# Optimization experiments

Measured on AMD Instinct MI355X. Metric: run time of the kernel, lower is better.

## Reference

```python
import jax, jax.numpy as jnp
import numpy as np

LATENT_DIM = 128
KQ_DIM = 32
B, N, K = 4, 16384, 64


def setup_inputs() -> dict:
    key = jax.random.key(0)
    k1, k2, k3, k4, k5, k6, k7 = jax.random.split(key, 7)
    return {
        "indices": jax.random.randint(k1, (3, B, N, K), 0, N, dtype=jnp.int64)
        if jax.config.jax_enable_x64 else jax.random.randint(k1, (3, B, N, K), 0, N, dtype=jnp.int32),
        "img": jax.random.normal(k2, (B, 3, 128, 128), dtype=jnp.float32),
        "features": jax.random.normal(k3, (B, N, LATENT_DIM), dtype=jnp.float32),
        "Wk": jax.random.normal(k4, (KQ_DIM, LATENT_DIM), dtype=jnp.float32) * 0.05,
        "bk": jax.random.normal(k5, (KQ_DIM,), dtype=jnp.float32) * 0.05,
        "Wq": jax.random.normal(k6, (KQ_DIM, LATENT_DIM), dtype=jnp.float32) * 0.05,
        "bq": jax.random.normal(k7, (KQ_DIM,), dtype=jnp.float32) * 0.05,
    }


def reference(indices, img, features, Wk, bk, Wq, bq):
    # features: [B, N, latent] -> keys/queries: [B, N, D]
    ks = jnp.einsum("bnl,dl->bnd", features, Wk) + bk
    qs = jnp.einsum("bnl,dl->bnd", features, Wq) + bq
    D = ks.shape[-1]
    # indices row 1 indexes keys, row 2 indexes queries (values in [0, N))
    x_idx = indices[1].reshape(B, N * K)  # [B, N*K]
    y_idx = indices[2].reshape(B, N * K)
    # gather along node axis: [B, N*K, D]
    x_feat = jnp.take_along_axis(ks, x_idx[:, :, None], axis=1)
    y_feat = jnp.take_along_axis(qs, y_idx[:, :, None], axis=1)
    # scaled dot product per edge -> [B, N, K]
    logits = (x_feat * y_feat).sum(axis=-1).reshape(B, N, K) * (D ** -0.5)
    return logits
```

## Files before the change

kernel.cpp:

```cpp
#include <hip/hip_runtime.h>
#include <hip/hip_fp16.h>

#define LATENT 128
#define DQK    32
#define BB     4
#define NN     16384
#define KK     64
#define TOTAL_EDGES (BB * NN * KK)
#define TOTAL_NODES (BB * NN)
#define PAD    132

__global__ __launch_bounds__(256, 2) void proj_kernel(
    const float* __restrict__ features,
    const float* __restrict__ Wk,
    const float* __restrict__ bk,
    const float* __restrict__ Wq,
    const float* __restrict__ bq,
    __half* __restrict__ ks,
    __half* __restrict__ qs)
{
    __shared__ float sf[64 * PAD];
    __shared__ float sw[64 * PAD];
    __shared__ float sb[64];

    const int t = threadIdx.x;
    const int node0 = blockIdx.x * 64;

    #pragma unroll
    for (int j = 0; j < 8; ++j) {
        int idx = t + j * 256;
        int r = idx >> 5;
        int c = idx & 31;
        const float4* src = (r < 32) ? (const float4*)Wk : (const float4*)Wq;
        float4 v = src[(size_t)(r & 31) * 32 + c];
        *(float4*)&sw[r * PAD + c * 4] = v;
    }
    if (t < 64) sb[t] = (t < 32) ? bk[t] : bq[t - 32];

    #pragma unroll
    for (int j = 0; j < 8; ++j) {
        int idx = t + j * 256;
        int r = idx >> 5;
        int c = idx & 31;
        float4 v = ((const float4*)(features + (size_t)(node0 + r) * LATENT))[c];
        *(float4*)&sf[r * PAD + c * 4] = v;
    }
    __syncthreads();

    const int tx = t & 15;
    const int ty = t >> 4;

    float acc[4][4];
    #pragma unroll
    for (int i = 0; i < 4; ++i)
        #pragma unroll
        for (int u = 0; u < 4; ++u) acc[i][u] = 0.f;

    #pragma unroll 4
    for (int kk = 0; kk < 32; ++kk) {
        float4 a[4], b[4];
        #pragma unroll
        for (int i = 0; i < 4; ++i)
            a[i] = *(const float4*)&sf[(ty * 4 + i) * PAD + kk * 4];
        #pragma unroll
        for (int u = 0; u < 4; ++u)
            b[u] = *(const float4*)&sw[(tx + 16 * u) * PAD + kk * 4];
        #pragma unroll
        for (int i = 0; i < 4; ++i)
            #pragma unroll
            for (int u = 0; u < 4; ++u)
                acc[i][u] += a[i].x * b[u].x + a[i].y * b[u].y
                           + a[i].z * b[u].z + a[i].w * b[u].w;
    }

    #pragma unroll
    for (int u = 0; u < 4; ++u) {
        const int d = tx + 16 * u;
        const float bias = sb[d];
        __half* base = (d < 32) ? ks : qs;
        const int dd = d & 31;
        #pragma unroll
        for (int i = 0; i < 4; ++i) {
            const int node = node0 + ty * 4 + i;
            base[(size_t)node * DQK + dd] = __float2half(acc[i][u] + bias);
        }
    }
}

__device__ __forceinline__ float dot8_h(uint4 a, uint4 b) {
    const __half2* ah = (const __half2*)&a;
    const __half2* bh = (const __half2*)&b;
    float s = 0.f;
    #pragma unroll
    for (int i = 0; i < 4; ++i) {
        const float2 af = __half22float2(ah[i]);
        const float2 bf = __half22float2(bh[i]);
        s += af.x * bf.x + af.y * bf.y;
    }
    return s;
}

__global__ __launch_bounds__(256) void edge_kernel(
    const int* __restrict__ xidx,
    const int* __restrict__ yidx,
    const __half* __restrict__ ks,
    const __half* __restrict__ qs,
    float* __restrict__ out)
{
    const int t = blockIdx.x * 256 + threadIdx.x;
    const int e = t >> 2;
    const int j = t & 3;
    const int b = e >> 20;

    const int x = xidx[e];
    const int y = yidx[e];

    const uint4 kv = ((const uint4*)ks)[((size_t)((b << 14) + x)) * 4 + j];
    const uint4 qv = ((const uint4*)qs)[((size_t)((b << 14) + y)) * 4 + j];

    float acc = dot8_h(kv, qv);
    acc += __shfl_xor(acc, 1);
    acc += __shfl_xor(acc, 2);

    if (j == 0) out[e] = acc * 0.17677669529663687f;
}

extern "C" void kernel_launch(void* const* d_in, const int* in_sizes, int n_in,
                              void* d_out, int out_size, void* d_ws, size_t ws_size,
                              hipStream_t stream) {
    const int*   indices  = (const int*)d_in[0];
    const float* features = (const float*)d_in[2];
    const float* Wk       = (const float*)d_in[3];
    const float* bk       = (const float*)d_in[4];
    const float* Wq       = (const float*)d_in[5];
    const float* bq       = (const float*)d_in[6];
    float* out = (float*)d_out;

    __half* ks = (__half*)d_ws;
    __half* qs = ks + (size_t)TOTAL_NODES * DQK;

    const int* xidx = indices + (size_t)1 * TOTAL_EDGES;
    const int* yidx = indices + (size_t)2 * TOTAL_EDGES;

    proj_kernel<<<TOTAL_NODES / 64, 256, 0, stream>>>(features, Wk, bk, Wq, bq, ks, qs);
    edge_kernel<<<(TOTAL_EDGES * 4) / 256, 256, 0, stream>>>(xidx, yidx, ks, qs, out);
}
```

Before: 74.12 us.

## Compute edge dot products with MFMA diagonal, one wave per 64 edges

Replaces the 4-threads-per-edge shuffle reduction with a 16x16x32 f16 MFMA per group of 16 edges, extracting the diagonal entries as the dot products. Each wave processes 64 edges in four unrolled groups, cutting launched threads by four and removing shuffles and conversions. It wastes most of the matrix product and adds a per-lane select, and fewer threads may hide gather latency less well.

```diff
diff --git a/kernel.cpp b/kernel.cpp
--- a/kernel.cpp
+++ b/kernel.cpp
@@ -9,6 +9,9 @@
 #define TOTAL_EDGES (BB * NN * KK)
 #define TOTAL_NODES (BB * NN)
 #define PAD    132
+
+typedef _Float16 half8 __attribute__((ext_vector_type(8)));
+typedef float    f32x4 __attribute__((ext_vector_type(4)));
 
 __global__ __launch_bounds__(256, 2) void proj_kernel(
     const float* __restrict__ features,
@@ -87,19 +90,6 @@
     }
 }
 
-__device__ __forceinline__ float dot8_h(uint4 a, uint4 b) {
-    const __half2* ah = (const __half2*)&a;
-    const __half2* bh = (const __half2*)&b;
-    float s = 0.f;
-    #pragma unroll
-    for (int i = 0; i < 4; ++i) {
-        const float2 af = __half22float2(ah[i]);
-        const float2 bf = __half22float2(bh[i]);
-        s += af.x * bf.x + af.y * bf.y;
-    }
-    return s;
-}
-
 __global__ __launch_bounds__(256) void edge_kernel(
     const int* __restrict__ xidx,
     const int* __restrict__ yidx,
@@ -107,22 +97,39 @@
     const __half* __restrict__ qs,
     float* __restrict__ out)
 {
-    const int t = blockIdx.x * 256 + threadIdx.x;
-    const int e = t >> 2;
-    const int j = t & 3;
-    const int b = e >> 20;
+    const int lane = threadIdx.x & 63;
+    const int wave = (blockIdx.x * 256 + threadIdx.x) >> 6;
+    const int i = lane & 15;
+    const int c = lane >> 4;
+    const int e_base = wave * 64;
+    const int b = e_base >> 20;
+    const int nodebase = b << 14;
 
-    const int x = xidx[e];
-    const int y = yidx[e];
+    const _Float16* ksh = (const _Float16*)ks;
+    const _Float16* qsh = (const _Float16*)qs;
 
-    const uint4 kv = ((const uint4*)ks)[((size_t)((b << 14) + x)) * 4 + j];
-    const uint4 qv = ((const uint4*)qs)[((size_t)((b << 14) + y)) * 4 + j];
+    const bool writer = (c == (i >> 2));
+    const int reg = i & 3;
 
-    float acc = dot8_h(kv, qv);
-    acc += __shfl_xor(acc, 1);
-    acc += __shfl_xor(acc, 2);
+    #pragma unroll
+    for (int g = 0; g < 4; ++g) {
+        const int e0 = e_base + g * 16;
+        const int x = xidx[e0 + i];
+        const int y = yidx[e0 + i];
 
-    if (j == 0) out[e] = acc * 0.17677669529663687f;
+        const half8 kv = *(const half8*)(ksh + (((size_t)(nodebase + x)) << 5) + (c << 3));
+        const half8 qv = *(const half8*)(qsh + (((size_t)(nodebase + y)) << 5) + (c << 3));
+
+        f32x4 acc = {0.f, 0.f, 0.f, 0.f};
+        acc = __builtin_amdgcn_mfma_f32_16x16x32_f16(kv, qv, acc, 0, 0, 0);
+
+        float v = acc[0];
+        v = (reg == 1) ? acc[1] : v;
+        v = (reg == 2) ? acc[2] : v;
+        v = (reg == 3) ? acc[3] : v;
+
+        if (writer) out[e0 + i] = v * 0.17677669529663687f;
+    }
 }
 
 extern "C" void kernel_launch(void* const* d_in, const int* in_sizes, int n_in,
@@ -143,5 +150,5 @@
     const int* yidx = indices + (size_t)2 * TOTAL_EDGES;
 
     proj_kernel<<<TOTAL_NODES / 64, 256, 0, stream>>>(features, Wk, bk, Wq, bq, ks, qs);
-    edge_kernel<<<(TOTAL_EDGES * 4) / 256, 256, 0, stream>>>(xidx, yidx, ks, qs, out);
+    edge_kernel<<<TOTAL_EDGES / 256, 256, 0, stream>>>(xidx, yidx, ks, qs, out);
 }
```

Result: slower. 78.17 us (+5.5%).

## Quantize keys/queries to int8 with per-node scales and restructure edge kernel

Applied to the files above, without the earlier changes.

The projection kernel now quantizes each node's key and query vectors to int8 using a per-node absmax scale stored in fp16, in place of writing fp16 vectors. The edge kernel assigns one edge per thread and processes four edges each. It loads the per-batch scales into shared memory, gathers 32-byte int8 rows, and computes dot products with sdot4 before rescaling. This halves gather bytes and removes cross-lane shuffles, at the cost of int8 quantization error that may exceed tolerance, and 64KB of LDS per block, which limits occupancy.

```diff
diff --git a/kernel.cpp b/kernel.cpp
--- a/kernel.cpp
+++ b/kernel.cpp
@@ -8,7 +8,20 @@
 #define KK     64
 #define TOTAL_EDGES (BB * NN * KK)
 #define TOTAL_NODES (BB * NN)
-#define PAD    132
+#define PADF   132
+#define EPT    4
+
+__device__ __forceinline__ int dot4i8(int a, int b, int c) {
+#if __has_builtin(__builtin_amdgcn_sdot4)
+    return __builtin_amdgcn_sdot4(a, b, c, false);
+#else
+    c += ((a << 24) >> 24) * ((b << 24) >> 24);
+    c += ((a << 16) >> 24) * ((b << 16) >> 24);
+    c += ((a <<  8) >> 24) * ((b <<  8) >> 24);
+    c += (a >> 24) * (b >> 24);
+    return c;
+#endif
+}
 
 __global__ __launch_bounds__(256, 2) void proj_kernel(
     const float* __restrict__ features,
@@ -16,11 +29,13 @@
     const float* __restrict__ bk,
     const float* __restrict__ Wq,
     const float* __restrict__ bq,
-    __half* __restrict__ ks,
-    __half* __restrict__ qs)
+    signed char* __restrict__ ks8,
+    signed char* __restrict__ qs8,
+    __half* __restrict__ sk,
+    __half* __restrict__ sq)
 {
-    __shared__ float sf[64 * PAD];
-    __shared__ float sw[64 * PAD];
+    __shared__ float sf[64 * PADF];
+    __shared__ float sw[64 * PADF];
     __shared__ float sb[64];
 
     const int t = threadIdx.x;
@@ -33,7 +48,7 @@
         int c = idx & 31;
         const float4* src = (r < 32) ? (const float4*)Wk : (const float4*)Wq;
         float4 v = src[(size_t)(r & 31) * 32 + c];
-        *(float4*)&sw[r * PAD + c * 4] = v;
+        *(float4*)&sw[r * PADF + c * 4] = v;
     }
     if (t < 64) sb[t] = (t < 32) ? bk[t] : bq[t - 32];
 
@@ -43,7 +58,7 @@
         int r = idx >> 5;
         int c = idx & 31;
         float4 v = ((const float4*)(features + (size_t)(node0 + r) * LATENT))[c];
-        *(float4*)&sf[r * PAD + c * 4] = v;
+        *(float4*)&sf[r * PADF + c * 4] = v;
     }
     __syncthreads();
 
@@ -61,10 +76,10 @@
         float4 a[4], b[4];
         #pragma unroll
         for (int i = 0; i < 4; ++i)
-            a[i] = *(const float4*)&sf[(ty * 4 + i) * PAD + kk * 4];
+            a[i] = *(const float4*)&sf[(ty * 4 + i) * PADF + kk * 4];
         #pragma unroll
         for (int u = 0; u < 4; ++u)
-            b[u] = *(const float4*)&sw[(tx + 16 * u) * PAD + kk * 4];
+            b[u] = *(const float4*)&sw[(tx + 16 * u) * PADF + kk * 4];
         #pragma unroll
         for (int i = 0; i < 4; ++i)
             #pragma unroll
@@ -73,56 +88,111 @@
                            + a[i].z * b[u].z + a[i].w * b[u].w;
     }
 
-    #pragma unroll
-    for (int u = 0; u < 4; ++u) {
-        const int d = tx + 16 * u;
-        const float bias = sb[d];
-        __half* base = (d < 32) ? ks : qs;
-        const int dd = d & 31;
+    float vk0[4], vk1[4], vq0[4], vq1[4], mk[4], mq[4];
+    #pragma unroll
+    for (int i = 0; i < 4; ++i) {
+        vk0[i] = acc[i][0] + sb[tx];
+        vk1[i] = acc[i][1] + sb[tx + 16];
+        vq0[i] = acc[i][2] + sb[tx + 32];
+        vq1[i] = acc[i][3] + sb[tx + 48];
+        mk[i] = fmaxf(fabsf(vk0[i]), fabsf(vk1[i]));
+        mq[i] = fmaxf(fabsf(vq0[i]), fabsf(vq1[i]));
+    }
+    #pragma unroll
+    for (int mask = 1; mask < 16; mask <<= 1) {
         #pragma unroll
         for (int i = 0; i < 4; ++i) {
-            const int node = node0 + ty * 4 + i;
-            base[(size_t)node * DQK + dd] = __float2half(acc[i][u] + bias);
+            mk[i] = fmaxf(mk[i], __shfl_xor(mk[i], mask));
+            mq[i] = fmaxf(mq[i], __shfl_xor(mq[i], mask));
         }
     }
-}
-
-__device__ __forceinline__ float dot8_h(uint4 a, uint4 b) {
-    const __half2* ah = (const __half2*)&a;
-    const __half2* bh = (const __half2*)&b;
-    float s = 0.f;
     #pragma unroll
     for (int i = 0; i < 4; ++i) {
-        const float2 af = __half22float2(ah[i]);
-        const float2 bf = __half22float2(bh[i]);
-        s += af.x * bf.x + af.y * bf.y;
-    }
-    return s;
-}
-
-__global__ __launch_bounds__(256) void edge_kernel(
+        const int node = node0 + ty * 4 + i;
+        const float invk = (mk[i] > 0.f) ? 127.f / mk[i] : 0.f;
+        const float invq = (mq[i] > 0.f) ? 127.f / mq[i] : 0.f;
+        signed char* kr = ks8 + (size_t)node * 32;
+        signed char* qr = qs8 + (size_t)node * 32;
+        kr[tx]      = (signed char)__float2int_rn(vk0[i] * invk);
+        kr[tx + 16] = (signed char)__float2int_rn(vk1[i] * invk);
+        qr[tx]      = (signed char)__float2int_rn(vq0[i] * invq);
+        qr[tx + 16] = (signed char)__float2int_rn(vq1[i] * invq);
+        if (tx == 0) {
+            sk[node] = __float2half(mk[i] * (1.f / 127.f));
+            sq[node] = __float2half(mq[i] * (1.f / 127.f));
+        }
+    }
+}
+
+__global__ __launch_bounds__(512, 2) void edge_kernel(
     const int* __restrict__ xidx,
     const int* __restrict__ yidx,
-    const __half* __restrict__ ks,
-    const __half* __restrict__ qs,
+    const signed char* __restrict__ ks8,
+    const signed char* __restrict__ qs8,
+    const __half* __restrict__ sk,
+    const __half* __restrict__ sq,
     float* __restrict__ out)
 {
-    const int t = blockIdx.x * 256 + threadIdx.x;
-    const int e = t >> 2;
-    const int j = t & 3;
-    const int b = e >> 20;
-
-    const int x = xidx[e];
-    const int y = yidx[e];
-
-    const uint4 kv = ((const uint4*)ks)[((size_t)((b << 14) + x)) * 4 + j];
-    const uint4 qv = ((const uint4*)qs)[((size_t)((b << 14) + y)) * 4 + j];
-
-    float acc = dot8_h(kv, qv);
-    acc += __shfl_xor(acc, 1);
-    acc += __shfl_xor(acc, 2);
-
-    if (j == 0) out[e] = acc * 0.17677669529663687f;
+    __shared__ __half ssk[NN];
+    __shared__ __half ssq[NN];
+
+    const int t = threadIdx.x;
+    const int b = blockIdx.x >> 9;
+
+    const uint4* gk = (const uint4*)(sk + (size_t)b * NN);
+    const uint4* gq = (const uint4*)(sq + (size_t)b * NN);
+    uint4* lk = (uint4*)ssk;
+    uint4* lq = (uint4*)ssq;
+    #pragma unroll
+    for (int j = 0; j < 4; ++j) {
+        lk[t + j * 512] = gk[t + j * 512];
+        lq[t + j * 512] = gq[t + j * 512];
+    }
+    __syncthreads();
+
+    const int base_e = (blockIdx.x & 511) * (512 * EPT);
+    const int gbase  = b << 20;
+    const size_t nodebase = (size_t)b << 14;
+
+    int xs[EPT], ys[EPT];
+    #pragma unroll
+    for (int m = 0; m < EPT; ++m) {
+        const int e = base_e + m * 512 + t;
+        xs[m] = xidx[gbase + e];
+        ys[m] = yidx[gbase + e];
+    }
+    __builtin_amdgcn_sched_barrier(0);
+
+    uint4 kv0[EPT], kv1[EPT], qv0[EPT], qv1[EPT];
+    const uint4* k4 = (const uint4*)ks8;
+    const uint4* q4 = (const uint4*)qs8;
+    #pragma unroll
+    for (int m = 0; m < EPT; ++m) {
+        const size_t xo = (nodebase + (size_t)xs[m]) << 1;
+        const size_t yo = (nodebase + (size_t)ys[m]) << 1;
+        kv0[m] = k4[xo];
+        kv1[m] = k4[xo + 1];
+        qv0[m] = q4[yo];
+        qv1[m] = q4[yo + 1];
+    }
+    __builtin_amdgcn_sched_barrier(0);
+
+    #pragma unroll
+    for (int m = 0; m < EPT; ++m) {
+        int d = 0;
+        d = dot4i8((int)kv0[m].x, (int)qv0[m].x, d);
+        d = dot4i8((int)kv0[m].y, (int)qv0[m].y, d);
+        d = dot4i8((int)kv0[m].z, (int)qv0[m].z, d);
+        d = dot4i8((int)kv0[m].w, (int)qv0[m].w, d);
+        d = dot4i8((int)kv1[m].x, (int)qv1[m].x, d);
+        d = dot4i8((int)kv1[m].y, (int)qv1[m].y, d);
+        d = dot4i8((int)kv1[m].z, (int)qv1[m].z, d);
+        d = dot4i8((int)kv1[m].w, (int)qv1[m].w, d);
+        const float skx = __half2float(ssk[xs[m]]);
+        const float sqy = __half2float(ssq[ys[m]]);
+        const int e = base_e + m * 512 + t;
+        out[gbase + e] = (float)d * skx * sqy * 0.17677669529663687f;
+    }
 }
 
 extern "C" void kernel_launch(void* const* d_in, const int* in_sizes, int n_in,
@@ -136,12 +206,15 @@
     const float* bq       = (const float*)d_in[6];
     float* out = (float*)d_out;
 
-    __half* ks = (__half*)d_ws;
-    __half* qs = ks + (size_t)TOTAL_NODES * DQK;
+    signed char* ks8 = (signed char*)d_ws;
+    signed char* qs8 = ks8 + (size_t)TOTAL_NODES * 32;
+    __half* sk = (__half*)(qs8 + (size_t)TOTAL_NODES * 32);
+    __half* sq = sk + TOTAL_NODES;
 
     const int* xidx = indices + (size_t)1 * TOTAL_EDGES;
     const int* yidx = indices + (size_t)2 * TOTAL_EDGES;
 
-    proj_kernel<<<TOTAL_NODES / 64, 256, 0, stream>>>(features, Wk, bk, Wq, bq, ks, qs);
-    edge_kernel<<<(TOTAL_EDGES * 4) / 256, 256, 0, stream>>>(xidx, yidx, ks, qs, out);
-}
+    proj_kernel<<<TOTAL_NODES / 64, 256, 0, stream>>>(
+        features, Wk, bk, Wq, bq, ks8, qs8, sk, sq);
+    edge_kernel<<<BB * 512, 512, 0, stream>>>(xidx, yidx, ks8, qs8, sk, sq, out);
+}
```

Result: no change. 74.24 us, median of 2 (+0.2%).
